# Optimization experiments

Measured on AMD Instinct MI355X. Metric: run time of the kernel, lower is better.

## Reference

```python
import jax, jax.numpy as jnp
import numpy as np
from jax import lax

B, T, H, OUT = 2048, 512, 128, 64  # batch, lookback, hidden, horizon


def _p(k, shape):
    return jax.random.normal(k, shape, jnp.float32) * 0.1


def setup_inputs() -> dict:
    key = jax.random.key(0)
    ks = jax.random.split(key, 19)
    d = {"x": jax.random.normal(ks[0], (B, T), jnp.float32)}
    i = 1
    for pre in ("enc", "dec"):
        for l in range(2):
            insz = 1 if l == 0 else H
            d[f"{pre}_Wih{l}"] = _p(ks[i], (4 * H, insz)); i += 1
            d[f"{pre}_Whh{l}"] = _p(ks[i], (4 * H, H)); i += 1
            d[f"{pre}_bih{l}"] = _p(ks[i], (4 * H,)); i += 1
            d[f"{pre}_bhh{l}"] = _p(ks[i], (4 * H,)); i += 1
    d["lin_W"] = _p(ks[17], (1, H))
    d["lin_b"] = _p(ks[18], (1,))
    return d


def _cell(x, h, c, Wih, Whh, bih, bhh):
    # PyTorch LSTM gate order: i, f, g, o
    gates = x @ Wih.T + h @ Whh.T + bih + bhh  # [B, 4H]
    i, f, g, o = jnp.split(gates, 4, axis=-1)
    c = jax.nn.sigmoid(f) * c + jax.nn.sigmoid(i) * jnp.tanh(g)
    h = jax.nn.sigmoid(o) * jnp.tanh(c)
    return h, c


def _layer(xs, Wih, Whh, bih, bhh):
    # xs: [T, B, in] -> (ys [T, B, H], final (h, c))
    b = xs.shape[1]
    h0 = jnp.zeros((b, Whh.shape[1]), xs.dtype)
    def step(carry, x):
        h, c = _cell(x, carry[0], carry[1], Wih, Whh, bih, bhh)
        return (h, c), h
    (h, c), ys = lax.scan(step, (h0, h0), xs)
    return ys, (h, c)


def reference(x,
              enc_Wih0, enc_Whh0, enc_bih0, enc_bhh0,
              enc_Wih1, enc_Whh1, enc_bih1, enc_bhh1,
              dec_Wih0, dec_Whh0, dec_bih0, dec_bhh0,
              dec_Wih1, dec_Whh1, dec_bih1, dec_bhh1,
              lin_W, lin_b):
    xs = x.T[:, :, None]  # [T, B, 1]
    ys0, (h0, c0) = _layer(xs, enc_Wih0, enc_Whh0, enc_bih0, enc_bhh0)
    _,   (h1, c1) = _layer(ys0, enc_Wih1, enc_Whh1, enc_bih1, enc_bhh1)

    inp0 = x[:, -1:]  # [B, 1] last observed price
    def dec_step(carry, _):
        inp, a, b_, h, c = carry
        a, b_ = _cell(inp, a, b_, dec_Wih0, dec_Whh0, dec_bih0, dec_bhh0)
        h, c = _cell(a, h, c, dec_Wih1, dec_Whh1, dec_bih1, dec_bhh1)
        pred = h @ lin_W.T + lin_b  # [B, 1]
        return (pred, a, b_, h, c), pred[:, 0]

    _, preds = lax.scan(dec_step, (inp0, h0, c0, h1, c1), None, length=OUT)
    return preds.T  # [B, OUT]
```

## Files before the change

### kernel.cpp

```cpp
#include <hip/hip_runtime.h>


typedef _Float16 half_t;
typedef _Float16 f16x8 __attribute__((ext_vector_type(8)));
typedef float    f32x4 __attribute__((ext_vector_type(4)));

#define BT   8
#define H    128
#define T    512
#define OUTS 64

__device__ __forceinline__ float sigm(float x)   { return 1.0f / (1.0f + __expf(-x)); }
__device__ __forceinline__ float tanh_f(float x) { return 2.0f / (1.0f + __expf(-2.0f * x)) - 1.0f; }

__device__ __forceinline__ void mfma_a(f32x4& d, f16x8 a, const f16x8& b) {
  asm("v_mfma_f32_16x16x32_f16 %0, %1, %2, %0" : "+v"(d) : "v"(a), "a"(b));
}
__device__ __forceinline__ void mfma_v(f32x4& d, f16x8 a, const f16x8& b) {
  asm("v_mfma_f32_16x16x32_f16 %0, %1, %2, %0" : "+v"(d) : "v"(a), "v"(b));
}

__device__ __forceinline__ f16x8 lda(const half_t* buf, int col, int kg, int kb) {
  int b  = col >> 1;
  int bc = (kb * 64 + kg * 16) ^ (b << 4);
  return *(const f16x8*)((const char*)buf + b * 256 + bc);
}

__device__ __forceinline__ void wr_h(half_t* hb, int b, int j, float h) {
  int bc = (j * 2) ^ (b << 4);
  *(half_t*)((char*)hb + b * 256 + bc) = (half_t)h;
}

template <int M>
__device__ __forceinline__ void pass_a(f32x4 (&acc)[2][4], const f16x8 (&wa)[2][4][2][4],
                                       const half_t* buf, int col, int kg) {
#pragma unroll
  for (int kb = 0; kb < 4; kb++) {
    f16x8 a = lda(buf, col, kg, kb);
#pragma unroll
    for (int jt = 0; jt < 2; jt++)
#pragma unroll
      for (int q = 0; q < 4; q++)
        mfma_a(acc[jt][q], a, wa[M][q][jt][kb]);
  }
}

__device__ __forceinline__ void pass_v(f32x4 (&acc)[2][4], const f16x8 (&wv2)[4][2][4],
                                       const half_t* buf, int col, int kg) {
#pragma unroll
  for (int kb = 0; kb < 4; kb++) {
    f16x8 a = lda(buf, col, kg, kb);
#pragma unroll
    for (int jt = 0; jt < 2; jt++)
#pragma unroll
      for (int q = 0; q < 4; q++)
        mfma_v(acc[jt][q], a, wv2[q][jt][kb]);
  }
}

__device__ __forceinline__ void zacc(f32x4 (&acc)[2][4]) {
#pragma unroll
  for (int jt = 0; jt < 2; jt++)
#pragma unroll
    for (int q = 0; q < 4; q++) acc[jt][q] = (f32x4){0.f, 0.f, 0.f, 0.f};
}

__device__ __forceinline__ void load_wa(f16x8 (&wa)[2][4][2][4], const half_t* w16,
                                        int base, int wv, int col, int kg) {
#pragma unroll
  for (int m = 0; m < 2; m++)
#pragma unroll
    for (int q = 0; q < 4; q++)
#pragma unroll
      for (int jt = 0; jt < 2; jt++)
#pragma unroll
        for (int kb = 0; kb < 4; kb++) {
          wa[m][q][jt][kb] = *(const f16x8*)(w16 + (size_t)(base + m) * 65536 +
                                             (size_t)(q * 128 + wv * 32 + jt * 16 + col) * 128 +
                                             kb * 32 + kg * 8);
          asm("" : "+a"(wa[m][q][jt][kb]));
        }
}

__device__ __forceinline__ void load_wv(f16x8 (&wv2)[4][2][4], const half_t* w16,
                                        int base, int wv, int col, int kg) {
#pragma unroll
  for (int q = 0; q < 4; q++)
#pragma unroll
    for (int jt = 0; jt < 2; jt++)
#pragma unroll
      for (int kb = 0; kb < 4; kb++)
        wv2[q][jt][kb] = *(const f16x8*)(w16 + (size_t)(base + 2) * 65536 +
                                         (size_t)(q * 128 + wv * 32 + jt * 16 + col) * 128 +
                                         kb * 32 + kg * 8);
}

__global__ void prep_kernel(const float* m0, const float* m1, const float* m2,
                            const float* m3, const float* m4, const float* m5,
                            const float* ba0, const float* bb0, const float* ba1, const float* bb1,
                            const float* ba2, const float* bb2, const float* ba3, const float* bb3,
                            const float* encWih0, const float* decWih0,
                            half_t* w16, float* biasT, float* xwT) {
  int i = blockIdx.x * 256 + threadIdx.x;
  if (i < 6 * 65536) {
    int m = i >> 16, e = i & 65535;
    const float* src = (m == 0) ? m0 : (m == 1) ? m1 : (m == 2) ? m2
                     : (m == 3) ? m3 : (m == 4) ? m4 : m5;
    w16[i] = (half_t)src[e];
  }
  if (i < 2048) {
    int set = i >> 9, wi = i & 511, q = wi >> 7, jh = wi & 127;
    const float* A  = (set == 0) ? ba0 : (set == 1) ? ba1 : (set == 2) ? ba2 : ba3;
    const float* Bv = (set == 0) ? bb0 : (set == 1) ? bb1 : (set == 2) ? bb2 : bb3;
    biasT[set * 512 + jh * 4 + q] = A[wi] + Bv[wi];
  }
  if (i < 1024) {
    int ph = i >> 9, wi = i & 511, q = wi >> 7, jh = wi & 127;
    xwT[ph * 512 + jh * 4 + q] = (ph ? decWih0 : encWih0)[wi];
  }
}

__global__ __launch_bounds__(256, 1)
void lstm_all(const float* __restrict__ x,
              const float* __restrict__ linW,
              const float* __restrict__ linb,
              const half_t* __restrict__ w16,
              const float* __restrict__ biasTg,
              const float* __restrict__ xwTg,
              float* __restrict__ out)
{
  __shared__ alignas(16) half_t h0b[2][BT * H];
  __shared__ alignas(16) half_t h1b[2][BT * H];
  __shared__ float xch[64 * BT];
  __shared__ float h1f[BT * H];
  __shared__ float linWs[H];
  __shared__ float pp[256];
  __shared__ float predbuf[BT];

  const int tid  = threadIdx.x;
  const int wv   = tid >> 6;
  const int lane = tid & 63;
  const int col  = lane & 15;
  const int kg   = lane >> 4;
  const int b0   = blockIdx.x * BT;

  for (int z = tid; z < 1024; z += 256) {
    ((unsigned*)h0b)[z] = 0u; ((unsigned*)h1b)[z] = 0u;
  }
  if (tid < H) linWs[tid] = linW[tid];

  f16x8 wa[2][4][2][4];
  f16x8 wv2[4][2][4];
  load_wa(wa, w16, 0, wv, col, kg);
  load_wv(wv2, w16, 0, wv, col, kg);

  float b0r[2][4], b1r[2][4], xwr[2][4];
#pragma unroll
  for (int jt = 0; jt < 2; jt++) {
    const int jj = wv * 32 + jt * 16 + col;
#pragma unroll
    for (int q = 0; q < 4; q++) {
      b0r[jt][q] = biasTg[jj * 4 + q];
      b1r[jt][q] = biasTg[512 + jj * 4 + q];
      xwr[jt][q] = xwTg[jj * 4 + q];
    }
  }

  float c0[2][2] = {{0, 0}, {0, 0}};
  float c1[2][2] = {{0, 0}, {0, 0}};

  for (int e = tid; e < BT * 64; e += 256) {
    int b = e >> 6, j = e & 63;
    xch[j * 8 + b] = x[(size_t)(b0 + b) * T + j];
  }
  __syncthreads();

  {
    f32x4 acc[2][4];
    zacc(acc);
    pass_a<0>(acc, wa, h0b[0], col, kg);
#pragma unroll
    for (int jt = 0; jt < 2; jt++) {
      const int jj = wv * 32 + jt * 16 + col;
#pragma unroll
      for (int s = 0; s < 2; s++) {
        const int b = 2 * kg + s;
        const int e = 2 * s;
        float xv = xch[0 * 8 + b];
        float gi = acc[jt][0][e] + b0r[jt][0] + xv * xwr[jt][0];
        float gf = acc[jt][1][e] + b0r[jt][1] + xv * xwr[jt][1];
        float gg = acc[jt][2][e] + b0r[jt][2] + xv * xwr[jt][2];
        float go = acc[jt][3][e] + b0r[jt][3] + xv * xwr[jt][3];
        float cn = sigm(gf) * c0[jt][s] + sigm(gi) * tanh_f(gg);
        c0[jt][s] = cn;
        wr_h(h0b[1], b, jj, sigm(go) * tanh_f(cn));
      }
    }
  }
  __syncthreads();
  int p = 1;

  for (int S = 0; S < 511; S++) {
    if (((S + 1) & 63) == 0) {
      const int ch = (S + 1) >> 6;
      for (int e = tid; e < BT * 64; e += 256) {
        int b = e >> 6, j = e & 63;
        xch[j * 8 + b] = x[(size_t)(b0 + b) * T + ch * 64 + j];
      }
      __syncthreads();
    }
    const int np = p ^ 1;
    f32x4 acc[2][4];
    zacc(acc);
    pass_v(acc, wv2, h1b[p], col, kg);
    pass_a<1>(acc, wa, h0b[p], col, kg);
#pragma unroll
    for (int jt = 0; jt < 2; jt++) {
      const int jj = wv * 32 + jt * 16 + col;
#pragma unroll
      for (int s = 0; s < 2; s++) {
        const int b = 2 * kg + s;
        const int e = 2 * s;
        float gi = acc[jt][0][e] + b1r[jt][0];
        float gf = acc[jt][1][e] + b1r[jt][1];
        float gg = acc[jt][2][e] + b1r[jt][2];
        float go = acc[jt][3][e] + b1r[jt][3];
        float cn = sigm(gf) * c1[jt][s] + sigm(gi) * tanh_f(gg);
        c1[jt][s] = cn;
        wr_h(h1b[np], b, jj, sigm(go) * tanh_f(cn));
      }
    }
    zacc(acc);
    pass_a<0>(acc, wa, h0b[p], col, kg);
#pragma unroll
    for (int jt = 0; jt < 2; jt++) {
      const int jj = wv * 32 + jt * 16 + col;
#pragma unroll
      for (int s = 0; s < 2; s++) {
        const int b = 2 * kg + s;
        const int e = 2 * s;
        float xv = xch[((S + 1) & 63) * 8 + b];
        float gi = acc[jt][0][e] + b0r[jt][0] + xv * xwr[jt][0];
        float gf = acc[jt][1][e] + b0r[jt][1] + xv * xwr[jt][1];
        float gg = acc[jt][2][e] + b0r[jt][2] + xv * xwr[jt][2];
        float go = acc[jt][3][e] + b0r[jt][3] + xv * xwr[jt][3];
        float cn = sigm(gf) * c0[jt][s] + sigm(gi) * tanh_f(gg);
        c0[jt][s] = cn;
        wr_h(h0b[np], b, jj, sigm(go) * tanh_f(cn));
      }
    }
    __syncthreads();
    p = np;
  }

  {
    const int np = p ^ 1;
    f32x4 acc[2][4];
    zacc(acc);
    pass_v(acc, wv2, h1b[p], col, kg);
    pass_a<1>(acc, wa, h0b[p], col, kg);
#pragma unroll
    for (int jt = 0; jt < 2; jt++) {
      const int jj = wv * 32 + jt * 16 + col;
#pragma unroll
      for (int s = 0; s < 2; s++) {
        const int b = 2 * kg + s;
        const int e = 2 * s;
        float gi = acc[jt][0][e] + b1r[jt][0];
        float gf = acc[jt][1][e] + b1r[jt][1];
        float gg = acc[jt][2][e] + b1r[jt][2];
        float go = acc[jt][3][e] + b1r[jt][3];
        float cn = sigm(gf) * c1[jt][s] + sigm(gi) * tanh_f(gg);
        c1[jt][s] = cn;
        wr_h(h1b[np], b, jj, sigm(go) * tanh_f(cn));
      }
    }
    __syncthreads();
  }
  int p0 = p;
  int p1 = p ^ 1;

  load_wa(wa, w16, 3, wv, col, kg);
  load_wv(wv2, w16, 3, wv, col, kg);
#pragma unroll
  for (int jt = 0; jt < 2; jt++) {
    const int jj = wv * 32 + jt * 16 + col;
#pragma unroll
    for (int q = 0; q < 4; q++) {
      b0r[jt][q] = biasTg[1024 + jj * 4 + q];
      b1r[jt][q] = biasTg[1536 + jj * 4 + q];
      xwr[jt][q] = xwTg[512 + jj * 4 + q];
    }
  }
  const float lb = linb[0];
  if (tid < BT) predbuf[tid] = x[(size_t)(b0 + tid) * T + (T - 1)];
  __syncthreads();

  for (int so = 0; so < OUTS; so++) {
    const int n0 = p0 ^ 1, n1 = p1 ^ 1;
    f32x4 acc[2][4];
    zacc(acc);
    pass_a<0>(acc, wa, h0b[p0], col, kg);
#pragma unroll
    for (int jt = 0; jt < 2; jt++) {
      const int jj = wv * 32 + jt * 16 + col;
#pragma unroll
      for (int s = 0; s < 2; s++) {
        const int b = 2 * kg + s;
        const int e = 2 * s;
        float xv = predbuf[b];
        float gi = acc[jt][0][e] + b0r[jt][0] + xv * xwr[jt][0];
        float gf = acc[jt][1][e] + b0r[jt][1] + xv * xwr[jt][1];
        float gg = acc[jt][2][e] + b0r[jt][2] + xv * xwr[jt][2];
        float go = acc[jt][3][e] + b0r[jt][3] + xv * xwr[jt][3];
        float cn = sigm(gf) * c0[jt][s] + sigm(gi) * tanh_f(gg);
        c0[jt][s] = cn;
        wr_h(h0b[n0], b, jj, sigm(go) * tanh_f(cn));
      }
    }
    __syncthreads();
    zacc(acc);
    pass_v(acc, wv2, h1b[p1], col, kg);
    pass_a<1>(acc, wa, h0b[n0], col, kg);
#pragma unroll
    for (int jt = 0; jt < 2; jt++) {
      const int jj = wv * 32 + jt * 16 + col;
#pragma unroll
      for (int s = 0; s < 2; s++) {
        const int b = 2 * kg + s;
        const int e = 2 * s;
        float cn = sigm(acc[jt][1][e] + b1r[jt][1]) * c1[jt][s]
                 + sigm(acc[jt][0][e] + b1r[jt][0]) * tanh_f(acc[jt][2][e] + b1r[jt][2]);
        c1[jt][s] = cn;
        float hn = sigm(acc[jt][3][e] + b1r[jt][3]) * tanh_f(cn);
        wr_h(h1b[n1], b, jj, hn);
        h1f[b * H + jj] = hn;
      }
    }
    __syncthreads();
    {
      int r = tid >> 5, seg = tid & 31;
      float pv = 0.0f;
#pragma unroll
      for (int kk = 0; kk < 4; kk++) pv += h1f[r * H + seg * 4 + kk] * linWs[seg * 4 + kk];
      pp[tid] = pv;
    }
    __syncthreads();
    if (tid < BT) {
      float pv = lb;
#pragma unroll
      for (int g2 = 0; g2 < 32; g2++) pv += pp[tid * 32 + g2];
      predbuf[tid] = pv;
      out[(size_t)(b0 + tid) * OUTS + so] = pv;
    }
    __syncthreads();
    p0 = n0; p1 = n1;
  }
}

extern "C" void kernel_launch(void* const* d_in, const int* in_sizes, int n_in,
                              void* d_out, int out_size, void* d_ws, size_t ws_size,
                              hipStream_t stream) {
  const float* x        = (const float*)d_in[0];
  const float* encWih0  = (const float*)d_in[1];
  const float* encWhh0  = (const float*)d_in[2];
  const float* encbih0  = (const float*)d_in[3];
  const float* encbhh0  = (const float*)d_in[4];
  const float* encWih1  = (const float*)d_in[5];
  const float* encWhh1  = (const float*)d_in[6];
  const float* encbih1  = (const float*)d_in[7];
  const float* encbhh1  = (const float*)d_in[8];
  const float* decWih0  = (const float*)d_in[9];
  const float* decWhh0  = (const float*)d_in[10];
  const float* decbih0  = (const float*)d_in[11];
  const float* decbhh0  = (const float*)d_in[12];
  const float* decWih1  = (const float*)d_in[13];
  const float* decWhh1  = (const float*)d_in[14];
  const float* decbih1  = (const float*)d_in[15];
  const float* decbhh1  = (const float*)d_in[16];
  const float* linW     = (const float*)d_in[17];
  const float* linb     = (const float*)d_in[18];

  half_t* w16  = (half_t*)d_ws;
  float*  biasT = (float*)((char*)d_ws + (size_t)6 * 65536 * 2);
  float*  xwT   = biasT + 2048;

  prep_kernel<<<1536, 256, 0, stream>>>(encWhh0, encWih1, encWhh1, decWhh0, decWih1, decWhh1,
                                        encbih0, encbhh0, encbih1, encbhh1,
                                        decbih0, decbhh0, decbih1, decbhh1,
                                        encWih0, decWih0, w16, biasT, xwT);
  lstm_all<<<256, 256, 0, stream>>>(x, linW, linb, w16, biasT, xwT, (float*)d_out);
}
```

Measured before the change: 1.313 ms.

## Split LSTM gate work across eight waves per block with per-wave weight slices

Adds a 512-thread variant of the fused LSTM kernel. Each of eight waves owns 16 hidden columns instead of 32, so per-wave MFMA work and register-held weight slices are halved, and step latency per batch tile should drop. A host-side occupancy and spill check picks the new kernel and falls back to the old one when it cannot run without scratch. The trade-off is more waves contending at each block-wide barrier, plus register pressure from holding three weight matrices in AGPRs.

```diff
diff --git a/kernel.cpp b/kernel.cpp
--- a/kernel.cpp
+++ b/kernel.cpp
@@ -93,6 +93,38 @@
         wv2[q][jt][kb] = *(const f16x8*)(w16 + (size_t)(base + 2) * 65536 +
                                          (size_t)(q * 128 + wv * 32 + jt * 16 + col) * 128 +
                                          kb * 32 + kg * 8);
+}
+
+template <int M>
+__device__ __forceinline__ void pass8(f32x4 (&acc)[4], const f16x8 (&wa)[3][4][4],
+                                      const half_t* buf, int col, int kg) {
+#pragma unroll
+  for (int kb = 0; kb < 4; kb++) {
+    f16x8 a = lda(buf, col, kg, kb);
+#pragma unroll
+    for (int q = 0; q < 4; q++)
+      mfma_a(acc[q], a, wa[M][q][kb]);
+  }
+}
+
+__device__ __forceinline__ void zacc8(f32x4 (&acc)[4]) {
+#pragma unroll
+  for (int q = 0; q < 4; q++) acc[q] = (f32x4){0.f, 0.f, 0.f, 0.f};
+}
+
+__device__ __forceinline__ void load_w8(f16x8 (&wa)[3][4][4], const half_t* w16,
+                                        int base, int wv, int col, int kg) {
+#pragma unroll
+  for (int m = 0; m < 3; m++)
+#pragma unroll
+    for (int q = 0; q < 4; q++)
+#pragma unroll
+      for (int kb = 0; kb < 4; kb++) {
+        wa[m][q][kb] = *(const f16x8*)(w16 + (size_t)(base + m) * 65536 +
+                                       (size_t)(q * 128 + wv * 16 + col) * 128 +
+                                       kb * 32 + kg * 8);
+        asm("" : "+a"(wa[m][q][kb]));
+      }
 }
 
 __global__ void prep_kernel(const float* m0, const float* m1, const float* m2,
@@ -121,12 +153,9 @@
 }
 
 __global__ __launch_bounds__(256, 1)
-void lstm_all(const float* __restrict__ x,
-              const float* __restrict__ linW,
-              const float* __restrict__ linb,
-              const half_t* __restrict__ w16,
-              const float* __restrict__ biasTg,
-              const float* __restrict__ xwTg,
+void lstm_all(const float* __restrict__ x, const float* __restrict__ linW,
+              const float* __restrict__ linb, const half_t* __restrict__ w16,
+              const float* __restrict__ biasTg, const float* __restrict__ xwTg,
               float* __restrict__ out)
 {
   __shared__ alignas(16) half_t h0b[2][BT * H];
@@ -339,6 +368,226 @@
     }
     __syncthreads();
     {
+      int r = tid >> 5, seg = tid & 31;
+      float pv = 0.0f;
+#pragma unroll
+      for (int kk = 0; kk < 4; kk++) pv += h1f[r * H + seg * 4 + kk] * linWs[seg * 4 + kk];
+      pp[tid] = pv;
+    }
+    __syncthreads();
+    if (tid < BT) {
+      float pv = lb;
+#pragma unroll
+      for (int g2 = 0; g2 < 32; g2++) pv += pp[tid * 32 + g2];
+      predbuf[tid] = pv;
+      out[(size_t)(b0 + tid) * OUTS + so] = pv;
+    }
+    __syncthreads();
+    p0 = n0; p1 = n1;
+  }
+}
+
+__global__ __launch_bounds__(512, 2)
+void lstm_all8(const float* __restrict__ x, const float* __restrict__ linW,
+               const float* __restrict__ linb, const half_t* __restrict__ w16,
+               const float* __restrict__ biasTg, const float* __restrict__ xwTg,
+               float* __restrict__ out)
+{
+  __shared__ alignas(16) half_t h0b[2][BT * H];
+  __shared__ alignas(16) half_t h1b[2][BT * H];
+  __shared__ float xch[64 * BT];
+  __shared__ float h1f[BT * H];
+  __shared__ float linWs[H];
+  __shared__ float pp[256];
+  __shared__ float predbuf[BT];
+
+  const int tid  = threadIdx.x;
+  const int wv   = tid >> 6;
+  const int lane = tid & 63;
+  const int col  = lane & 15;
+  const int kg   = lane >> 4;
+  const int b0   = blockIdx.x * BT;
+
+  for (int z = tid; z < 1024; z += 512) {
+    ((unsigned*)h0b)[z] = 0u; ((unsigned*)h1b)[z] = 0u;
+  }
+  if (tid < H) linWs[tid] = linW[tid];
+
+  f16x8 wa[3][4][4];
+  load_w8(wa, w16, 0, wv, col, kg);
+
+  float b0r[4], b1r[4], xwr[4];
+  {
+    const int jj = wv * 16 + col;
+#pragma unroll
+    for (int q = 0; q < 4; q++) {
+      b0r[q] = biasTg[jj * 4 + q];
+      b1r[q] = biasTg[512 + jj * 4 + q];
+      xwr[q] = xwTg[jj * 4 + q];
+    }
+  }
+
+  float c0[2] = {0, 0};
+  float c1[2] = {0, 0};
+
+  for (int e = tid; e < BT * 64; e += 512) {
+    int b = e >> 6, j = e & 63;
+    xch[j * 8 + b] = x[(size_t)(b0 + b) * T + j];
+  }
+  __syncthreads();
+
+  {
+    f32x4 acc[4];
+    zacc8(acc);
+    pass8<0>(acc, wa, h0b[0], col, kg);
+    const int jj = wv * 16 + col;
+#pragma unroll
+    for (int s = 0; s < 2; s++) {
+      const int b = 2 * kg + s;
+      const int e = 2 * s;
+      float xv = xch[0 * 8 + b];
+      float gi = acc[0][e] + b0r[0] + xv * xwr[0];
+      float gf = acc[1][e] + b0r[1] + xv * xwr[1];
+      float gg = acc[2][e] + b0r[2] + xv * xwr[2];
+      float go = acc[3][e] + b0r[3] + xv * xwr[3];
+      float cn = sigm(gf) * c0[s] + sigm(gi) * tanh_f(gg);
+      c0[s] = cn;
+      wr_h(h0b[1], b, jj, sigm(go) * tanh_f(cn));
+    }
+  }
+  __syncthreads();
+  int p = 1;
+
+  for (int S = 0; S < 511; S++) {
+    if (((S + 1) & 63) == 0) {
+      const int ch = (S + 1) >> 6;
+      for (int e = tid; e < BT * 64; e += 512) {
+        int b = e >> 6, j = e & 63;
+        xch[j * 8 + b] = x[(size_t)(b0 + b) * T + ch * 64 + j];
+      }
+      __syncthreads();
+    }
+    const int np = p ^ 1;
+    f32x4 acc[4];
+    zacc8(acc);
+    pass8<2>(acc, wa, h1b[p], col, kg);
+    pass8<1>(acc, wa, h0b[p], col, kg);
+    {
+      const int jj = wv * 16 + col;
+#pragma unroll
+      for (int s = 0; s < 2; s++) {
+        const int b = 2 * kg + s;
+        const int e = 2 * s;
+        float gi = acc[0][e] + b1r[0];
+        float gf = acc[1][e] + b1r[1];
+        float gg = acc[2][e] + b1r[2];
+        float go = acc[3][e] + b1r[3];
+        float cn = sigm(gf) * c1[s] + sigm(gi) * tanh_f(gg);
+        c1[s] = cn;
+        wr_h(h1b[np], b, jj, sigm(go) * tanh_f(cn));
+      }
+    }
+    zacc8(acc);
+    pass8<0>(acc, wa, h0b[p], col, kg);
+    {
+      const int jj = wv * 16 + col;
+#pragma unroll
+      for (int s = 0; s < 2; s++) {
+        const int b = 2 * kg + s;
+        const int e = 2 * s;
+        float xv = xch[((S + 1) & 63) * 8 + b];
+        float gi = acc[0][e] + b0r[0] + xv * xwr[0];
+        float gf = acc[1][e] + b0r[1] + xv * xwr[1];
+        float gg = acc[2][e] + b0r[2] + xv * xwr[2];
+        float go = acc[3][e] + b0r[3] + xv * xwr[3];
+        float cn = sigm(gf) * c0[s] + sigm(gi) * tanh_f(gg);
+        c0[s] = cn;
+        wr_h(h0b[np], b, jj, sigm(go) * tanh_f(cn));
+      }
+    }
+    __syncthreads();
+    p = np;
+  }
+
+  {
+    const int np = p ^ 1;
+    f32x4 acc[4];
+    zacc8(acc);
+    pass8<2>(acc, wa, h1b[p], col, kg);
+    pass8<1>(acc, wa, h0b[p], col, kg);
+    const int jj = wv * 16 + col;
+#pragma unroll
+    for (int s = 0; s < 2; s++) {
+      const int b = 2 * kg + s;
+      const int e = 2 * s;
+      float gi = acc[0][e] + b1r[0];
+      float gf = acc[1][e] + b1r[1];
+      float gg = acc[2][e] + b1r[2];
+      float go = acc[3][e] + b1r[3];
+      float cn = sigm(gf) * c1[s] + sigm(gi) * tanh_f(gg);
+      c1[s] = cn;
+      wr_h(h1b[np], b, jj, sigm(go) * tanh_f(cn));
+    }
+    __syncthreads();
+  }
+  int p0 = p;
+  int p1 = p ^ 1;
+
+  load_w8(wa, w16, 3, wv, col, kg);
+  {
+    const int jj = wv * 16 + col;
+#pragma unroll
+    for (int q = 0; q < 4; q++) {
+      b0r[q] = biasTg[1024 + jj * 4 + q];
+      b1r[q] = biasTg[1536 + jj * 4 + q];
+      xwr[q] = xwTg[512 + jj * 4 + q];
+    }
+  }
+  const float lb = linb[0];
+  if (tid < BT) predbuf[tid] = x[(size_t)(b0 + tid) * T + (T - 1)];
+  __syncthreads();
+
+  for (int so = 0; so < OUTS; so++) {
+    const int n0 = p0 ^ 1, n1 = p1 ^ 1;
+    f32x4 acc[4];
+    zacc8(acc);
+    pass8<0>(acc, wa, h0b[p0], col, kg);
+    {
+      const int jj = wv * 16 + col;
+#pragma unroll
+      for (int s = 0; s < 2; s++) {
+        const int b = 2 * kg + s;
+        const int e = 2 * s;
+        float xv = predbuf[b];
+        float gi = acc[0][e] + b0r[0] + xv * xwr[0];
+        float gf = acc[1][e] + b0r[1] + xv * xwr[1];
+        float gg = acc[2][e] + b0r[2] + xv * xwr[2];
+        float go = acc[3][e] + b0r[3] + xv * xwr[3];
+        float cn = sigm(gf) * c0[s] + sigm(gi) * tanh_f(gg);
+        c0[s] = cn;
+        wr_h(h0b[n0], b, jj, sigm(go) * tanh_f(cn));
+      }
+    }
+    __syncthreads();
+    zacc8(acc);
+    pass8<2>(acc, wa, h1b[p1], col, kg);
+    pass8<1>(acc, wa, h0b[n0], col, kg);
+    {
+      const int jj = wv * 16 + col;
+#pragma unroll
+      for (int s = 0; s < 2; s++) {
+        const int b = 2 * kg + s;
+        const int e = 2 * s;
+        float cn = sigm(acc[1][e] + b1r[1]) * c1[s]
+                 + sigm(acc[0][e] + b1r[0]) * tanh_f(acc[2][e] + b1r[2]);
+        c1[s] = cn;
+        float hn = sigm(acc[3][e] + b1r[3]) * tanh_f(cn);
+        wr_h(h1b[n1], b, jj, hn);
+        h1f[b * H + jj] = hn;
+      }
+    }
+    __syncthreads();
+    if (tid < 256) {
       int r = tid >> 5, seg = tid & 31;
       float pv = 0.0f;
 #pragma unroll
@@ -389,5 +638,18 @@
                                         encbih0, encbhh0, encbih1, encbhh1,
                                         decbih0, decbhh0, decbih1, decbhh1,
                                         encWih0, decWih0, w16, biasT, xwT);
-  lstm_all<<<256, 256, 0, stream>>>(x, linW, linb, w16, biasT, xwT, (float*)d_out);
-}
+
+  static int use8 = -1;
+  if (use8 < 0) {
+    hipFuncAttributes attr{};
+    int occ = 0;
+    hipError_t e1 = hipFuncGetAttributes(&attr, (const void*)lstm_all8);
+    hipError_t e2 = hipOccupancyMaxActiveBlocksPerMultiprocessor(&occ, (const void*)lstm_all8,
+                                                                 512, 0);
+    use8 = (e1 == hipSuccess && e2 == hipSuccess && occ >= 1 && attr.localSizeBytes == 0) ? 1 : 0;
+  }
+  if (use8)
+    lstm_all8<<<256, 512, 0, stream>>>(x, linW, linb, w16, biasT, xwT, (float*)d_out);
+  else
+    lstm_all<<<256, 256, 0, stream>>>(x, linW, linb, w16, biasT, xwT, (float*)d_out);
+}
```

Result: no change. 1.311 ms (-0.1%).
